# Optimization experiments

Hardware: AMD Instinct MI355X
Metric: run time of the kernel (lower is better)

The kernel has to match this reference:

```python
import jax, jax.numpy as jnp
import numpy as np

NUM_HEADS = 16
EPS = 1e-5


def _ln(x, w, b):
    mu = jnp.mean(x, axis=-1, keepdims=True)
    var = jnp.mean((x - mu) ** 2, axis=-1, keepdims=True)
    return (x - mu) * jax.lax.rsqrt(var + EPS) * w + b


def _ada_ln(x, vol, lw, lb, gamma, beta, vs_w, vs_b):
    y = _ln(x, lw, lb)
    # volatility_scale: Linear(1,1) on vol[..., None] -> sigmoid
    vs = jax.nn.sigmoid(vol[..., None] * vs_w + vs_b)  # (B,S,1)
    return y * (1.0 + vs) * gamma + beta


def setup_inputs() -> dict:
    key = jax.random.key(0)
    ks = jax.random.split(key, 20)
    B, S, H = 8, 1024, 1024
    Hf = 4 * H
    Hg = H // 2
    w = lambda k, i, o: jax.random.normal(k, (i, o), jnp.float32) * 0.02
    inp = {
        'x': jax.random.normal(ks[0], (B, S, H), jnp.float32),
        'volatility': jax.random.uniform(ks[1], (B, S), jnp.float32),
        'Wq': w(ks[2], H, H), 'bq': jnp.zeros((H,), jnp.float32),
        'Wk': w(ks[3], H, H), 'bk': jnp.zeros((H,), jnp.float32),
        'Wv': w(ks[4], H, H), 'bv': jnp.zeros((H,), jnp.float32),
        'Wo': w(ks[5], H, H), 'bo': jnp.zeros((H,), jnp.float32),
        'ln1_w': jnp.ones((H,), jnp.float32), 'ln1_b': jnp.zeros((H,), jnp.float32),
        'gamma1': jnp.ones((), jnp.float32), 'beta1': jnp.zeros((), jnp.float32),
        'vs1_w': jnp.float32(0.3), 'vs1_b': jnp.float32(0.0),
        'ffn_w1': w(ks[6], H, Hf), 'ffn_b1': jnp.zeros((Hf,), jnp.float32),
        'ffn_w2': w(ks[7], Hf, H), 'ffn_b2': jnp.zeros((H,), jnp.float32),
        'gate_w1': w(ks[8], H, Hg), 'gate_b1': jnp.zeros((Hg,), jnp.float32),
        'gate_w2': w(ks[9], Hg, H), 'gate_b2': jnp.zeros((H,), jnp.float32),
        'ln2_w': jnp.ones((H,), jnp.float32), 'ln2_b': jnp.zeros((H,), jnp.float32),
        'gamma2': jnp.ones((), jnp.float32), 'beta2': jnp.zeros((), jnp.float32),
        'vs2_w': jnp.float32(0.3), 'vs2_b': jnp.float32(0.0),
    }
    return inp


def reference(x, volatility, Wq, bq, Wk, bk, Wv, bv, Wo, bo,
              ln1_w, ln1_b, gamma1, beta1, vs1_w, vs1_b,
              ffn_w1, ffn_b1, ffn_w2, ffn_b2,
              gate_w1, gate_b1, gate_w2, gate_b2,
              ln2_w, ln2_b, gamma2, beta2, vs2_w, vs2_b):
    B, S, H = x.shape
    nh = NUM_HEADS
    hd = H // nh
    scale = np.sqrt(hd).astype(np.float32)

    # self-attention (eval mode -> dropout is identity)
    Q = (x @ Wq + bq).reshape(B, S, nh, hd)
    K = (x @ Wk + bk).reshape(B, S, nh, hd)
    V = (x @ Wv + bv).reshape(B, S, nh, hd)
    scores = jnp.einsum('bqhd,bkhd->bhqk', Q, K) / scale
    attn = jax.nn.softmax(scores, axis=-1)
    ctx = jnp.einsum('bhqk,bkhd->bqhd', attn, V).reshape(B, S, H)
    attn_out = ctx @ Wo + bo

    x = x + attn_out
    x = _ada_ln(x, volatility, ln1_w, ln1_b, gamma1, beta1, vs1_w, vs1_b)

    # volatility-adaptive FFN (volatility present -> gated path)
    h = jax.nn.gelu(x @ ffn_w1 + ffn_b1, approximate=False)
    ffn_out = h @ ffn_w2 + ffn_b2
    g = jax.nn.sigmoid(jax.nn.relu(x @ gate_w1 + gate_b1) @ gate_w2 + gate_b2)
    ffn_res = ffn_out * g + x * (1.0 - g)

    x = x + ffn_res
    x = _ada_ln(x, volatility, ln2_w, ln2_b, gamma2, beta2, vs2_w, vs2_b)
    return x
```

## Files before the change

### kernel.cpp

```cpp
#include <hip/hip_runtime.h>
#include <hip/hip_bf16.h>
#include <math.h>


#define HDIM 1024
#define NHEAD 16
#define DHEAD 64
#define NBATCH 8
#define NSEQ 1024
#define NTOK (NBATCH * NSEQ)
#define QKVSTR 3072
#define LNEPS 1e-5f
#define LOG2E_8 0.180336880f

using f32x4 = __attribute__((ext_vector_type(4))) float;
using s16x8 = __attribute__((ext_vector_type(8))) short;
using u16x8 = __attribute__((ext_vector_type(8))) unsigned short;

enum { ACT_NONE = 0, ACT_GELU = 1, ACT_RELU = 2, ACT_SIG = 3 };

__device__ inline float bf2f(unsigned short u) {
    union { unsigned u; float f; } t; t.u = ((unsigned)u) << 16; return t.f;
}
__device__ inline unsigned short f2bf(float f) {
    __hip_bfloat16 h = __float2bfloat16(f);
    return *reinterpret_cast<unsigned short*>(&h);
}
__device__ inline float gelu_f(float t) {
    const float u = t * (0.7978845608f + 0.0356774081f * t * t);
    const float e = __expf(2.f * u);
    const float th = 1.f - 2.f / (e + 1.f);
    return 0.5f * t * (1.f + th);
}

#define GLDS16(g, l) __builtin_amdgcn_global_load_lds( \
    (__attribute__((address_space(1))) void*)(g),      \
    (__attribute__((address_space(3))) void*)(l), 16, 0, 0)
#define MFMA16(a, b, c) __builtin_amdgcn_mfma_f32_16x16x32_bf16(a, b, c, 0, 0, 0)
#define BAR() __builtin_amdgcn_s_barrier()
#define LGKM0() do { asm volatile("s_waitcnt lgkmcnt(0)" ::: "memory"); \
                     __builtin_amdgcn_sched_barrier(0); } while (0)

template<int N> __device__ __forceinline__ void vmwait() {
    asm volatile("s_waitcnt vmcnt(%0)" :: "i"(N) : "memory");
}

__global__ __launch_bounds__(256)
void cast_bf16_k(const float* __restrict__ in, unsigned short* __restrict__ out, int n4)
{
    for (int i = blockIdx.x * 256 + threadIdx.x; i < n4; i += gridDim.x * 256) {
        float4 v = ((const float4*)in)[i];
        ushort4 o;
        o.x = f2bf(v.x); o.y = f2bf(v.y); o.z = f2bf(v.z); o.w = f2bf(v.w);
        ((ushort4*)out)[i] = o;
    }
}

__global__ __launch_bounds__(256)
void concat3_k(const float* __restrict__ a, const float* __restrict__ b,
               const float* __restrict__ c, float* __restrict__ o)
{
    int i = blockIdx.x * 256 + threadIdx.x;
    o[i] = i < 1024 ? a[i] : (i < 2048 ? b[i - 1024] : c[i - 2048]);
}

__global__ __launch_bounds__(256)
void transpose_cast_k(const float* __restrict__ W, unsigned short* __restrict__ Wt,
                      int K, int N)
{
    __shared__ float tile[32][33];
    const int tx = threadIdx.x, ty = threadIdx.y;
    const int k0 = blockIdx.y * 32, n0 = blockIdx.x * 32;
#pragma unroll
    for (int r = 0; r < 32; r += 8)
        tile[ty + r][tx] = W[(size_t)(k0 + ty + r) * N + n0 + tx];
    __syncthreads();
#pragma unroll
    for (int r = 0; r < 32; r += 8)
        Wt[(size_t)(n0 + ty + r) * K + k0 + tx] = f2bf(tile[tx][ty + r]);
}

__global__ __launch_bounds__(256)
void transpose_cast4_k(const float* __restrict__ W0, const float* __restrict__ W1,
                       const float* __restrict__ W2, const float* __restrict__ W3,
                       unsigned short* __restrict__ Wt)
{
    __shared__ float tile[32][33];
    const int z = blockIdx.z;
    const float* W = z == 0 ? W0 : z == 1 ? W1 : z == 2 ? W2 : W3;
    unsigned short* dst = Wt + (size_t)z * HDIM * HDIM;
    const int tx = threadIdx.x, ty = threadIdx.y;
    const int k0 = blockIdx.y * 32, n0 = blockIdx.x * 32;
#pragma unroll
    for (int r = 0; r < 32; r += 8)
        tile[ty + r][tx] = W[(size_t)(k0 + ty + r) * HDIM + n0 + tx];
    __syncthreads();
#pragma unroll
    for (int r = 0; r < 32; r += 8)
        dst[(size_t)(n0 + ty + r) * HDIM + k0 + tx] = f2bf(tile[tx][ty + r]);
}

__global__ __launch_bounds__(256)
void transpose_v_k(const unsigned short* __restrict__ vb, unsigned short* __restrict__ vtb)
{
    __shared__ unsigned short t[64][72];
    const int tid = threadIdx.x;
    const int b = blockIdx.z, h = blockIdx.y;
    const int s0 = blockIdx.x * 64;
    {
        const int r = tid >> 3, c = (tid & 7) * 8;
        *(u16x8*)&t[r][c] =
            *(const u16x8*)&vb[((size_t)(b * NSEQ + s0 + r)) * QKVSTR + h * DHEAD + c];
        *(u16x8*)&t[r + 32][c] =
            *(const u16x8*)&vb[((size_t)(b * NSEQ + s0 + r + 32)) * QKVSTR + h * DHEAD + c];
    }
    __syncthreads();
    {
        const int d = tid & 63, sc = (tid >> 6) * 16;
        u16x8 o0, o1;
#pragma unroll
        for (int i = 0; i < 8; ++i) o0[i] = t[sc + i][d];
#pragma unroll
        for (int i = 0; i < 8; ++i) o1[i] = t[sc + 8 + i][d];
        unsigned short* dst = &vtb[((size_t)((b * NHEAD + h) * DHEAD + d)) * NSEQ + s0 + sc];
        *(u16x8*)dst = o0;
        *(u16x8*)(dst + 8) = o1;
    }
}

template<int ACT, bool HAS_ADD, bool OUT_BF>
__global__ __launch_bounds__(256, 4)
void gemm_hi_k(const unsigned short* __restrict__ A, const unsigned short* __restrict__ Bt,
               const float* __restrict__ bias, const float* __restrict__ add,
               void* __restrict__ Cv, int M, int N, int K, int nbx)
{
    __shared__ alignas(16) unsigned short As[2][128 * 32];
    __shared__ alignas(16) unsigned short Bs[2][128 * 32];

    const int tid = threadIdx.x;
    const int lane = tid & 63;
    const int w = tid >> 6;
    const int wr = w >> 1, wc = w & 1;
    const int chunk = gridDim.x >> 3;
    const int wg = (blockIdx.x & 7) * chunk + (blockIdx.x >> 3);
    const int m0 = (wg / nbx) * 128;
    const int n0 = (wg % nbx) * 128;

    const int fr = lane & 15;
    const int fo = lane >> 4;
    const int fo_swz8 = (fo ^ ((fr >> 1) & 3)) * 8;

    const int srow = tid >> 2;
    const int sg8 = ((tid & 3) ^ ((tid >> 3) & 3)) * 8;

    f32x4 acc[4][4] = {};

    auto stage = [&](int t) {
        const int buf = t & 1;
        const unsigned short* as_ = A + (size_t)(m0 + srow) * K + t * 32 + sg8;
        const unsigned short* bs_ = Bt + (size_t)(n0 + srow) * K + t * 32 + sg8;
        GLDS16(as_, &As[buf][(w * 16) * 32]);
        GLDS16(as_ + (size_t)64 * K, &As[buf][(64 + w * 16) * 32]);
        GLDS16(bs_, &Bs[buf][(w * 16) * 32]);
        GLDS16(bs_ + (size_t)64 * K, &Bs[buf][(64 + w * 16) * 32]);
    };

    const int NT = K / 32;
    stage(0);

    for (int t = 0; t < NT; ++t) {
        if (t + 1 < NT) { stage(t + 1); vmwait<4>(); }
        else            { vmwait<0>(); }
        BAR();

        const int buf = t & 1;
        s16x8 af[4], bf[4];
#pragma unroll
        for (int i = 0; i < 4; ++i)
            af[i] = *(const s16x8*)(&As[buf][(wr * 64 + i * 16 + fr) * 32 + fo_swz8]);
#pragma unroll
        for (int j = 0; j < 4; ++j)
            bf[j] = *(const s16x8*)(&Bs[buf][(wc * 64 + j * 16 + fr) * 32 + fo_swz8]);

        __builtin_amdgcn_s_setprio(1);
#pragma unroll
        for (int i = 0; i < 4; ++i)
#pragma unroll
            for (int j = 0; j < 4; ++j)
                acc[i][j] = MFMA16(af[i], bf[j], acc[i][j]);
        __builtin_amdgcn_s_setprio(0);

        LGKM0();
        BAR();
    }

    float bv[4];
#pragma unroll
    for (int j = 0; j < 4; ++j)
        bv[j] = bias[n0 + wc * 64 + j * 16 + fr];
#pragma unroll
    for (int i = 0; i < 4; ++i) {
#pragma unroll
        for (int j = 0; j < 4; ++j) {
            const int gn = n0 + wc * 64 + j * 16 + fr;
#pragma unroll
            for (int r = 0; r < 4; ++r) {
                const int gm = m0 + wr * 64 + i * 16 + fo * 4 + r;
                float t = acc[i][j][r] + bv[j];
                if (HAS_ADD) t += add[(size_t)gm * N + gn];
                if (ACT == ACT_GELU)      t = gelu_f(t);
                else if (ACT == ACT_RELU) t = fmaxf(t, 0.f);
                else if (ACT == ACT_SIG)  t = 1.f / (1.f + __expf(-t));
                if (OUT_BF) ((unsigned short*)Cv)[(size_t)gm * N + gn] = f2bf(t);
                else        ((float*)Cv)[(size_t)gm * N + gn] = t;
            }
        }
    }
}

__global__ __launch_bounds__(512, 6)
void attn_k(const unsigned short* __restrict__ QKVb, const unsigned short* __restrict__ Vtb,
            unsigned short* __restrict__ Cb)
{
    __shared__ alignas(16) unsigned short Ks[2][64 * 64];
    __shared__ alignas(16) unsigned short Vs[2][64 * 64];
    __shared__ alignas(16) unsigned short Ps[8][16 * 72];

    const int tid = threadIdx.x;
    const int lane = tid & 63;
    const int wid = tid >> 6;
    const int L = blockIdx.x;
    const int xcd = L & 7, s = L >> 3;
    const int bh = xcd + ((s >> 3) << 3);
    const int qt = s & 7;
    const int b = bh >> 4, h = bh & 15;
    const int q0 = qt * 128 + wid * 16;

    const int kcol = lane & 15;
    const int kofs = (lane >> 4) * 8;
    const size_t qoff = ((size_t)(b * NSEQ + q0 + kcol)) * QKVSTR + h * DHEAD + kofs;
    const s16x8 qf0 = *(const s16x8*)(QKVb + qoff);
    const s16x8 qf1 = *(const s16x8*)(QKVb + qoff + 32);

    f32x4 accO[4] = {};
    float mrow[4] = {-1e30f, -1e30f, -1e30f, -1e30f};
    float lsum[4] = {0.f, 0.f, 0.f, 0.f};

    const int lr = lane >> 3;
    const int swz8 = (((lane & 7) ^ lr)) * 8;
    const size_t kbase  = ((size_t)(b * NSEQ)) * QKVSTR + HDIM + h * DHEAD;
    const size_t vtbase = ((size_t)(bh * DHEAD)) * NSEQ;

    unsigned short* const pw = &Ps[wid][0];
    const int prow = (lane >> 4) * 4;

    auto stage = [&](int kt, int buf) {
        const int rowb = wid * 8;
        GLDS16(QKVb + kbase + (size_t)(kt * 64 + rowb + lr) * QKVSTR + swz8,
               Ks[buf] + rowb * 64);
        GLDS16(Vtb + vtbase + (size_t)(rowb + lr) * NSEQ + kt * 64 + swz8,
               Vs[buf] + rowb * 64);
    };

    stage(0, 0);
    asm volatile("s_waitcnt vmcnt(0)" ::: "memory");
    __syncthreads();

    for (int kt = 0; kt < NSEQ / 64; ++kt) {
        const int cur = kt & 1;
        if (kt + 1 < NSEQ / 64) stage(kt + 1, cur ^ 1);

        f32x4 sa[4];
#pragma unroll
        for (int jt = 0; jt < 4; ++jt) {
            const int kr = jt * 16 + kcol;
            const unsigned swz = ((unsigned)(kr & 7)) << 4;
            const s16x8 kf0 = *(const s16x8*)((const char*)Ks[cur] + kr * 128 + ((kofs * 2) ^ swz));
            const s16x8 kf1 = *(const s16x8*)((const char*)Ks[cur] + kr * 128 + ((64 + kofs * 2) ^ swz));
            f32x4 t = {};
            t = MFMA16(qf0, kf0, t);
            t = MFMA16(qf1, kf1, t);
            sa[jt] = t * LOG2E_8;
        }

        float lmax[4];
#pragma unroll
        for (int r = 0; r < 4; ++r)
            lmax[r] = fmaxf(fmaxf(sa[0][r], sa[1][r]), fmaxf(sa[2][r], sa[3][r]));
        const float guard = fmaxf(fmaxf(lmax[0] - mrow[0], lmax[1] - mrow[1]),
                                  fmaxf(lmax[2] - mrow[2], lmax[3] - mrow[3]));
        if (!__all(guard <= 8.f)) {
#pragma unroll
            for (int r = 0; r < 4; ++r) {
                float m = lmax[r];
                m = fmaxf(m, __shfl_xor(m, 1));
                m = fmaxf(m, __shfl_xor(m, 2));
                m = fmaxf(m, __shfl_xor(m, 4));
                m = fmaxf(m, __shfl_xor(m, 8));
                const float mn = fmaxf(mrow[r], m);
                const float corr = exp2f(mrow[r] - mn);
                mrow[r] = mn;
                lsum[r] *= corr;
#pragma unroll
                for (int dt = 0; dt < 4; ++dt) accO[dt][r] *= corr;
            }
        }
#pragma unroll
        for (int r = 0; r < 4; ++r) {
#pragma unroll
            for (int jt = 0; jt < 4; ++jt) {
                const float p = exp2f(sa[jt][r] - mrow[r]);
                pw[(prow + r) * 72 + jt * 16 + kcol] = f2bf(p);
                lsum[r] += p;
            }
        }

#pragma unroll
        for (int kc = 0; kc < 2; ++kc) {
            const s16x8 pa = *(const s16x8*)(pw + kcol * 72 + kc * 32 + kofs);
#pragma unroll
            for (int dt = 0; dt < 4; ++dt) {
                const int dr = dt * 16 + kcol;
                const unsigned swz = ((unsigned)(dr & 7)) << 4;
                const s16x8 vf = *(const s16x8*)((const char*)Vs[cur] + dr * 128 +
                                                 ((kc * 64 + kofs * 2) ^ swz));
                accO[dt] = MFMA16(pa, vf, accO[dt]);
            }
        }

        if (kt + 1 < NSEQ / 64) asm volatile("s_waitcnt vmcnt(0)" ::: "memory");
        __builtin_amdgcn_s_barrier();
    }

#pragma unroll
    for (int r = 0; r < 4; ++r) {
        lsum[r] += __shfl_xor(lsum[r], 1);
        lsum[r] += __shfl_xor(lsum[r], 2);
        lsum[r] += __shfl_xor(lsum[r], 4);
        lsum[r] += __shfl_xor(lsum[r], 8);
    }

    const size_t obase = ((size_t)(b * NSEQ + q0 + prow)) * HDIM + h * DHEAD;
#pragma unroll
    for (int r = 0; r < 4; ++r) {
        const float rl = 1.f / lsum[r];
#pragma unroll
        for (int dt = 0; dt < 4; ++dt)
            Cb[obase + (size_t)r * HDIM + dt * 16 + kcol] = f2bf(accO[dt][r] * rl);
    }
}

template<int MODE, bool WRITE_BF>
__global__ __launch_bounds__(256)
void adaln_k(const float* __restrict__ a, const float* __restrict__ fo,
             const float* __restrict__ g, const float* __restrict__ vol,
             const float* __restrict__ lw, const float* __restrict__ lb,
             const float* __restrict__ gm, const float* __restrict__ bt,
             const float* __restrict__ vsw, const float* __restrict__ vsb,
             float* __restrict__ out, unsigned short* __restrict__ out_bf)
{
    const int tok = blockIdx.x;
    const int tid = threadIdx.x;
    const size_t base = (size_t)tok * HDIM + tid * 4;
    float v[4];
    {
        float4 va = *(const float4*)&a[base];
        if (MODE == 1) {
            float4 vf = *(const float4*)&fo[base];
            float4 vg = *(const float4*)&g[base];
            v[0] = va.x * (2.f - vg.x) + vf.x * vg.x;
            v[1] = va.y * (2.f - vg.y) + vf.y * vg.y;
            v[2] = va.z * (2.f - vg.z) + vf.z * vg.z;
            v[3] = va.w * (2.f - vg.w) + vf.w * vg.w;
        } else {
            v[0] = va.x; v[1] = va.y; v[2] = va.z; v[3] = va.w;
        }
    }
    float sum = v[0] + v[1] + v[2] + v[3];
    float sq  = v[0]*v[0] + v[1]*v[1] + v[2]*v[2] + v[3]*v[3];
#pragma unroll
    for (int off = 32; off > 0; off >>= 1) {
        sum += __shfl_down(sum, off);
        sq  += __shfl_down(sq, off);
    }
    __shared__ float ssum[4], ssq[4];
    const int wid = tid >> 6, lane = tid & 63;
    if (lane == 0) { ssum[wid] = sum; ssq[wid] = sq; }
    __syncthreads();
    const float tsum = ssum[0] + ssum[1] + ssum[2] + ssum[3];
    const float tsq  = ssq[0]  + ssq[1]  + ssq[2]  + ssq[3];
    const float mu   = tsum * (1.f / 1024.f);
    const float var  = tsq * (1.f / 1024.f) - mu * mu;
    const float rstd = rsqrtf(var + LNEPS);
    const float vsv  = 1.f / (1.f + __expf(-(vol[tok] * vsw[0] + vsb[0])));
    const float sca  = (1.f + vsv) * gm[0];
    const float off2 = bt[0];
    const float4 lwv = *(const float4*)&lw[tid * 4];
    const float4 lbv = *(const float4*)&lb[tid * 4];
    float r0 = ((v[0] - mu) * rstd * lwv.x + lbv.x) * sca + off2;
    float r1 = ((v[1] - mu) * rstd * lwv.y + lbv.y) * sca + off2;
    float r2 = ((v[2] - mu) * rstd * lwv.z + lbv.z) * sca + off2;
    float r3 = ((v[3] - mu) * rstd * lwv.w + lbv.w) * sca + off2;
    *(float4*)&out[base] = make_float4(r0, r1, r2, r3);
    if (WRITE_BF) {
        ushort4 ob;
        ob.x = f2bf(r0); ob.y = f2bf(r1); ob.z = f2bf(r2); ob.w = f2bf(r3);
        *(ushort4*)&out_bf[base] = ob;
    }
}

extern "C" void kernel_launch(void* const* d_in, const int* in_sizes, int n_in,
                              void* d_out, int out_size, void* d_ws, size_t ws_size,
                              hipStream_t stream)
{
    (void)in_sizes; (void)n_in; (void)out_size; (void)ws_size;
    const float* x    = (const float*)d_in[0];
    const float* vol  = (const float*)d_in[1];
    const float* Wq   = (const float*)d_in[2];  const float* bq  = (const float*)d_in[3];
    const float* Wk   = (const float*)d_in[4];  const float* bk  = (const float*)d_in[5];
    const float* Wv   = (const float*)d_in[6];  const float* bv  = (const float*)d_in[7];
    const float* Wo   = (const float*)d_in[8];  const float* bo  = (const float*)d_in[9];
    const float* ln1w = (const float*)d_in[10]; const float* ln1b = (const float*)d_in[11];
    const float* gm1  = (const float*)d_in[12]; const float* be1 = (const float*)d_in[13];
    const float* vs1w = (const float*)d_in[14]; const float* vs1b = (const float*)d_in[15];
    const float* fw1  = (const float*)d_in[16]; const float* fb1 = (const float*)d_in[17];
    const float* fw2  = (const float*)d_in[18]; const float* fb2 = (const float*)d_in[19];
    const float* gw1  = (const float*)d_in[20]; const float* gb1 = (const float*)d_in[21];
    const float* gw2  = (const float*)d_in[22]; const float* gb2 = (const float*)d_in[23];
    const float* ln2w = (const float*)d_in[24]; const float* ln2b = (const float*)d_in[25];
    const float* gm2  = (const float*)d_in[26]; const float* be2 = (const float*)d_in[27];
    const float* vs2w = (const float*)d_in[28]; const float* vs2b = (const float*)d_in[29];

    char* w = (char*)d_ws;
    auto MB = [](size_t v) { return v << 20; };
    unsigned short* wtqkv = (unsigned short*)(w + MB(0));
    unsigned short* wto   = (unsigned short*)(w + MB(6));
    unsigned short* wtf1  = (unsigned short*)(w + MB(8));
    unsigned short* wtf2  = (unsigned short*)(w + MB(16));
    unsigned short* wtg1  = (unsigned short*)(w + MB(24));
    unsigned short* wtg2  = (unsigned short*)(w + MB(25));
    unsigned short* xb   = (unsigned short*)(w + MB(26));
    unsigned short* qkvb = (unsigned short*)(w + MB(42));
    unsigned short* vtb  = (unsigned short*)(w + MB(90));
    unsigned short* cxb  = (unsigned short*)(w + MB(106));
    float*          ao   = (float*)(w + MB(122));
    float*          x1   = (float*)(w + MB(42));
    unsigned short* x1b  = (unsigned short*)(w + MB(74));
    unsigned short* hb   = (unsigned short*)(w + MB(90));
    float*          ffn  = (float*)(w + MB(154));
    unsigned short* ghb  = (unsigned short*)(w + MB(26));
    float*          gg   = (float*)(w + MB(90));
    float*          bqkv = (float*)(w + MB(186));

    dim3 blk(256);
    dim3 tb(32, 8);
    transpose_cast4_k<<<dim3(32, 32, 4), tb, 0, stream>>>(Wq, Wk, Wv, Wo, wtqkv);
    transpose_cast_k<<<dim3(4096/32, 1024/32), tb, 0, stream>>>(fw1, wtf1, 1024, 4096);
    transpose_cast_k<<<dim3(1024/32, 4096/32), tb, 0, stream>>>(fw2, wtf2, 4096, 1024);
    transpose_cast_k<<<dim3(512/32, 1024/32),  tb, 0, stream>>>(gw1, wtg1, 1024, 512);
    transpose_cast_k<<<dim3(1024/32, 512/32),  tb, 0, stream>>>(gw2, wtg2, 512, 1024);
    cast_bf16_k<<<2048, blk, 0, stream>>>(x, xb, NTOK * HDIM / 4);
    concat3_k<<<12, blk, 0, stream>>>(bq, bk, bv, bqkv);

    gemm_hi_k<ACT_NONE, false, true><<<dim3(24 * 64), blk, 0, stream>>>(
        xb, wtqkv, bqkv, nullptr, qkvb, NTOK, QKVSTR, HDIM, 24);
    transpose_v_k<<<dim3(NSEQ / 64, NHEAD, NBATCH), blk, 0, stream>>>(qkvb + 2048, vtb);
    attn_k<<<dim3(1024), 512, 0, stream>>>(qkvb, vtb, cxb);
    gemm_hi_k<ACT_NONE, true, false><<<dim3(8 * 64), blk, 0, stream>>>(
        cxb, wto, bo, x, ao, NTOK, HDIM, HDIM, 8);
    adaln_k<0, true><<<dim3(NTOK), blk, 0, stream>>>(
        ao, nullptr, nullptr, vol, ln1w, ln1b, gm1, be1, vs1w, vs1b, x1, x1b);
    gemm_hi_k<ACT_GELU, false, true><<<dim3(32 * 64), blk, 0, stream>>>(
        x1b, wtf1, fb1, nullptr, hb, NTOK, 4096, HDIM, 32);
    gemm_hi_k<ACT_NONE, false, false><<<dim3(8 * 64), blk, 0, stream>>>(
        hb, wtf2, fb2, nullptr, ffn, NTOK, HDIM, 4096, 8);
    gemm_hi_k<ACT_RELU, false, true><<<dim3(4 * 64), blk, 0, stream>>>(
        x1b, wtg1, gb1, nullptr, ghb, NTOK, 512, HDIM, 4);
    gemm_hi_k<ACT_SIG, false, false><<<dim3(8 * 64), blk, 0, stream>>>(
        ghb, wtg2, gb2, nullptr, gg, NTOK, HDIM, 512, 8);
    adaln_k<1, false><<<dim3(NTOK), blk, 0, stream>>>(
        x1, ffn, gg, vol, ln2w, ln2b, gm2, be2, vs2w, vs2b, (float*)d_out, nullptr);
}
```

Before: 469.4 us.

## Fuse FFN-up and gate-up GEMMs, store FFN and gate outputs in bf16

```diff
diff --git a/kernel.cpp b/kernel.cpp
--- a/kernel.cpp
+++ b/kernel.cpp
@@ -17,7 +17,7 @@
 using s16x8 = __attribute__((ext_vector_type(8))) short;
 using u16x8 = __attribute__((ext_vector_type(8))) unsigned short;
 
-enum { ACT_NONE = 0, ACT_GELU = 1, ACT_RELU = 2, ACT_SIG = 3 };
+enum { ACT_NONE = 0, ACT_GELU = 1, ACT_RELU = 2, ACT_SIG = 3, ACT_GR = 4 };
 
 __device__ inline float bf2f(unsigned short u) {
     union { unsigned u; float f; } t; t.u = ((unsigned)u) << 16; return t.f;
@@ -62,6 +62,14 @@
 {
     int i = blockIdx.x * 256 + threadIdx.x;
     o[i] = i < 1024 ? a[i] : (i < 2048 ? b[i - 1024] : c[i - 2048]);
+}
+
+__global__ __launch_bounds__(256)
+void concat2_k(const float* __restrict__ a, const float* __restrict__ b,
+               float* __restrict__ o)
+{
+    int i = blockIdx.x * 256 + threadIdx.x;
+    o[i] = i < 4096 ? a[i] : b[i - 4096];
 }
 
 __global__ __launch_bounds__(256)
@@ -129,10 +137,10 @@
 }
 
 template<int ACT, bool HAS_ADD, bool OUT_BF>
-__global__ __launch_bounds__(256, 4)
+__global__ __launch_bounds__(256, 5)
 void gemm_hi_k(const unsigned short* __restrict__ A, const unsigned short* __restrict__ Bt,
                const float* __restrict__ bias, const float* __restrict__ add,
-               void* __restrict__ Cv, int M, int N, int K, int nbx)
+               void* __restrict__ Cv, int M, int N, int K, int lda, int nbx)
 {
     __shared__ alignas(16) unsigned short As[2][128 * 32];
     __shared__ alignas(16) unsigned short Bs[2][128 * 32];
@@ -157,10 +165,10 @@
 
     auto stage = [&](int t) {
         const int buf = t & 1;
-        const unsigned short* as_ = A + (size_t)(m0 + srow) * K + t * 32 + sg8;
+        const unsigned short* as_ = A + (size_t)(m0 + srow) * lda + t * 32 + sg8;
         const unsigned short* bs_ = Bt + (size_t)(n0 + srow) * K + t * 32 + sg8;
         GLDS16(as_, &As[buf][(w * 16) * 32]);
-        GLDS16(as_ + (size_t)64 * K, &As[buf][(64 + w * 16) * 32]);
+        GLDS16(as_ + (size_t)64 * lda, &As[buf][(64 + w * 16) * 32]);
         GLDS16(bs_, &Bs[buf][(w * 16) * 32]);
         GLDS16(bs_ + (size_t)64 * K, &Bs[buf][(64 + w * 16) * 32]);
     };
@@ -211,6 +219,7 @@
                 if (ACT == ACT_GELU)      t = gelu_f(t);
                 else if (ACT == ACT_RELU) t = fmaxf(t, 0.f);
                 else if (ACT == ACT_SIG)  t = 1.f / (1.f + __expf(-t));
+                else if (ACT == ACT_GR)   t = (gn < 4096) ? gelu_f(t) : fmaxf(t, 0.f);
                 if (OUT_BF) ((unsigned short*)Cv)[(size_t)gm * N + gn] = f2bf(t);
                 else        ((float*)Cv)[(size_t)gm * N + gn] = t;
             }
@@ -352,8 +361,10 @@
 
 template<int MODE, bool WRITE_BF>
 __global__ __launch_bounds__(256)
-void adaln_k(const float* __restrict__ a, const float* __restrict__ fo,
-             const float* __restrict__ g, const float* __restrict__ vol,
+void adaln_k(const float* __restrict__ a,
+             const unsigned short* __restrict__ fo_bf,
+             const unsigned short* __restrict__ g_bf,
+             const float* __restrict__ vol,
              const float* __restrict__ lw, const float* __restrict__ lb,
              const float* __restrict__ gm, const float* __restrict__ bt,
              const float* __restrict__ vsw, const float* __restrict__ vsb,
@@ -366,12 +377,14 @@
     {
         float4 va = *(const float4*)&a[base];
         if (MODE == 1) {
-            float4 vf = *(const float4*)&fo[base];
-            float4 vg = *(const float4*)&g[base];
-            v[0] = va.x * (2.f - vg.x) + vf.x * vg.x;
-            v[1] = va.y * (2.f - vg.y) + vf.y * vg.y;
-            v[2] = va.z * (2.f - vg.z) + vf.z * vg.z;
-            v[3] = va.w * (2.f - vg.w) + vf.w * vg.w;
+            ushort4 uf = *(const ushort4*)&fo_bf[base];
+            ushort4 ug = *(const ushort4*)&g_bf[base];
+            float f0 = bf2f(uf.x), f1 = bf2f(uf.y), f2 = bf2f(uf.z), f3 = bf2f(uf.w);
+            float g0 = bf2f(ug.x), g1 = bf2f(ug.y), g2 = bf2f(ug.z), g3 = bf2f(ug.w);
+            v[0] = va.x * (2.f - g0) + f0 * g0;
+            v[1] = va.y * (2.f - g1) + f1 * g1;
+            v[2] = va.z * (2.f - g2) + f2 * g2;
+            v[3] = va.w * (2.f - g3) + f3 * g3;
         } else {
             v[0] = va.x; v[1] = va.y; v[2] = va.z; v[3] = va.w;
         }
@@ -435,9 +448,9 @@
     auto MB = [](size_t v) { return v << 20; };
     unsigned short* wtqkv = (unsigned short*)(w + MB(0));
     unsigned short* wto   = (unsigned short*)(w + MB(6));
-    unsigned short* wtf1  = (unsigned short*)(w + MB(8));
-    unsigned short* wtf2  = (unsigned short*)(w + MB(16));
-    unsigned short* wtg1  = (unsigned short*)(w + MB(24));
+    unsigned short* wtfg  = (unsigned short*)(w + MB(8));
+    unsigned short* wtg1  = (unsigned short*)(w + MB(16));
+    unsigned short* wtf2  = (unsigned short*)(w + MB(17));
     unsigned short* wtg2  = (unsigned short*)(w + MB(25));
     unsigned short* xb   = (unsigned short*)(w + MB(26));
     unsigned short* qkvb = (unsigned short*)(w + MB(42));
@@ -446,38 +459,37 @@
     float*          ao   = (float*)(w + MB(122));
     float*          x1   = (float*)(w + MB(42));
     unsigned short* x1b  = (unsigned short*)(w + MB(74));
-    unsigned short* hb   = (unsigned short*)(w + MB(90));
-    float*          ffn  = (float*)(w + MB(154));
-    unsigned short* ghb  = (unsigned short*)(w + MB(26));
-    float*          gg   = (float*)(w + MB(90));
-    float*          bqkv = (float*)(w + MB(186));
+    unsigned short* hgb  = (unsigned short*)(w + MB(90));
+    unsigned short* ffnb = (unsigned short*)(w + MB(162));
+    unsigned short* ggb  = (unsigned short*)(w + MB(26));
+    float*          bqkv = (float*)(w + MB(184));
+    float*          bfg  = (float*)(w + MB(185));
 
     dim3 blk(256);
     dim3 tb(32, 8);
     transpose_cast4_k<<<dim3(32, 32, 4), tb, 0, stream>>>(Wq, Wk, Wv, Wo, wtqkv);
-    transpose_cast_k<<<dim3(4096/32, 1024/32), tb, 0, stream>>>(fw1, wtf1, 1024, 4096);
+    transpose_cast_k<<<dim3(4096/32, 1024/32), tb, 0, stream>>>(fw1, wtfg, 1024, 4096);
+    transpose_cast_k<<<dim3(512/32, 1024/32),  tb, 0, stream>>>(gw1, wtg1, 1024, 512);
     transpose_cast_k<<<dim3(1024/32, 4096/32), tb, 0, stream>>>(fw2, wtf2, 4096, 1024);
-    transpose_cast_k<<<dim3(512/32, 1024/32),  tb, 0, stream>>>(gw1, wtg1, 1024, 512);
     transpose_cast_k<<<dim3(1024/32, 512/32),  tb, 0, stream>>>(gw2, wtg2, 512, 1024);
     cast_bf16_k<<<2048, blk, 0, stream>>>(x, xb, NTOK * HDIM / 4);
     concat3_k<<<12, blk, 0, stream>>>(bq, bk, bv, bqkv);
+    concat2_k<<<18, blk, 0, stream>>>(fb1, gb1, bfg);
 
     gemm_hi_k<ACT_NONE, false, true><<<dim3(24 * 64), blk, 0, stream>>>(
-        xb, wtqkv, bqkv, nullptr, qkvb, NTOK, QKVSTR, HDIM, 24);
+        xb, wtqkv, bqkv, nullptr, qkvb, NTOK, QKVSTR, HDIM, HDIM, 24);
     transpose_v_k<<<dim3(NSEQ / 64, NHEAD, NBATCH), blk, 0, stream>>>(qkvb + 2048, vtb);
     attn_k<<<dim3(1024), 512, 0, stream>>>(qkvb, vtb, cxb);
     gemm_hi_k<ACT_NONE, true, false><<<dim3(8 * 64), blk, 0, stream>>>(
-        cxb, wto, bo, x, ao, NTOK, HDIM, HDIM, 8);
+        cxb, wto, bo, x, ao, NTOK, HDIM, HDIM, HDIM, 8);
     adaln_k<0, true><<<dim3(NTOK), blk, 0, stream>>>(
         ao, nullptr, nullptr, vol, ln1w, ln1b, gm1, be1, vs1w, vs1b, x1, x1b);
-    gemm_hi_k<ACT_GELU, false, true><<<dim3(32 * 64), blk, 0, stream>>>(
-        x1b, wtf1, fb1, nullptr, hb, NTOK, 4096, HDIM, 32);
-    gemm_hi_k<ACT_NONE, false, false><<<dim3(8 * 64), blk, 0, stream>>>(
-        hb, wtf2, fb2, nullptr, ffn, NTOK, HDIM, 4096, 8);
-    gemm_hi_k<ACT_RELU, false, true><<<dim3(4 * 64), blk, 0, stream>>>(
-        x1b, wtg1, gb1, nullptr, ghb, NTOK, 512, HDIM, 4);
-    gemm_hi_k<ACT_SIG, false, false><<<dim3(8 * 64), blk, 0, stream>>>(
-        ghb, wtg2, gb2, nullptr, gg, NTOK, HDIM, 512, 8);
+    gemm_hi_k<ACT_GR, false, true><<<dim3(36 * 64), blk, 0, stream>>>(
+        x1b, wtfg, bfg, nullptr, hgb, NTOK, 4608, HDIM, HDIM, 36);
+    gemm_hi_k<ACT_NONE, false, true><<<dim3(8 * 64), blk, 0, stream>>>(
+        hgb, wtf2, fb2, nullptr, ffnb, NTOK, HDIM, 4096, 4608, 8);
+    gemm_hi_k<ACT_SIG, false, true><<<dim3(8 * 64), blk, 0, stream>>>(
+        hgb + 4096, wtg2, gb2, nullptr, ggb, NTOK, HDIM, 512, 4608, 8);
     adaln_k<1, false><<<dim3(NTOK), blk, 0, stream>>>(
-        x1, ffn, gg, vol, ln2w, ln2b, gm2, be2, vs2w, vs2b, (float*)d_out, nullptr);
-}
+        x1, ffnb, ggb, vol, ln2w, ln2b, gm2, be2, vs2w, vs2b, (float*)d_out, nullptr);
+}
```

New measurement: 686.9 us. +46.3%, slower.

## Use 64-row GEMM tiles for narrow-N GEMMs and store FFN/gate outputs as bf16

Applied to the files above, without the earlier changes.

```diff
diff --git a/kernel.cpp b/kernel.cpp
--- a/kernel.cpp
+++ b/kernel.cpp
@@ -128,22 +128,26 @@
     }
 }
 
-template<int ACT, bool HAS_ADD, bool OUT_BF>
+template<int BM, int ACT, bool HAS_ADD, bool OUT_BF>
 __global__ __launch_bounds__(256, 4)
 void gemm_hi_k(const unsigned short* __restrict__ A, const unsigned short* __restrict__ Bt,
                const float* __restrict__ bias, const float* __restrict__ add,
                void* __restrict__ Cv, int M, int N, int K, int nbx)
 {
-    __shared__ alignas(16) unsigned short As[2][128 * 32];
+    constexpr int NREP = (BM == 128) ? 4 : 2;
+    constexpr int AR = BM / 64;
+    constexpr int VM = AR + 2;
+    __shared__ alignas(16) unsigned short As[2][BM * 32];
     __shared__ alignas(16) unsigned short Bs[2][128 * 32];
 
     const int tid = threadIdx.x;
     const int lane = tid & 63;
     const int w = tid >> 6;
-    const int wr = w >> 1, wc = w & 1;
+    const int wr = (BM == 128) ? (w >> 1) : 0;
+    const int wcb = (BM == 128) ? ((w & 1) * 64) : (w * 32);
     const int chunk = gridDim.x >> 3;
     const int wg = (blockIdx.x & 7) * chunk + (blockIdx.x >> 3);
-    const int m0 = (wg / nbx) * 128;
+    const int m0 = (wg / nbx) * BM;
     const int n0 = (wg % nbx) * 128;
 
     const int fr = lane & 15;
@@ -153,14 +157,15 @@
     const int srow = tid >> 2;
     const int sg8 = ((tid & 3) ^ ((tid >> 3) & 3)) * 8;
 
-    f32x4 acc[4][4] = {};
+    f32x4 acc[4][NREP] = {};
 
     auto stage = [&](int t) {
         const int buf = t & 1;
         const unsigned short* as_ = A + (size_t)(m0 + srow) * K + t * 32 + sg8;
         const unsigned short* bs_ = Bt + (size_t)(n0 + srow) * K + t * 32 + sg8;
         GLDS16(as_, &As[buf][(w * 16) * 32]);
-        GLDS16(as_ + (size_t)64 * K, &As[buf][(64 + w * 16) * 32]);
+        if constexpr (BM == 128)
+            GLDS16(as_ + (size_t)64 * K, &As[buf][(64 + w * 16) * 32]);
         GLDS16(bs_, &Bs[buf][(w * 16) * 32]);
         GLDS16(bs_ + (size_t)64 * K, &Bs[buf][(64 + w * 16) * 32]);
     };
@@ -169,24 +174,24 @@
     stage(0);
 
     for (int t = 0; t < NT; ++t) {
-        if (t + 1 < NT) { stage(t + 1); vmwait<4>(); }
+        if (t + 1 < NT) { stage(t + 1); vmwait<VM>(); }
         else            { vmwait<0>(); }
         BAR();
 
         const int buf = t & 1;
-        s16x8 af[4], bf[4];
+        s16x8 af[4], bf[NREP];
 #pragma unroll
         for (int i = 0; i < 4; ++i)
             af[i] = *(const s16x8*)(&As[buf][(wr * 64 + i * 16 + fr) * 32 + fo_swz8]);
 #pragma unroll
-        for (int j = 0; j < 4; ++j)
-            bf[j] = *(const s16x8*)(&Bs[buf][(wc * 64 + j * 16 + fr) * 32 + fo_swz8]);
+        for (int j = 0; j < NREP; ++j)
+            bf[j] = *(const s16x8*)(&Bs[buf][(wcb + j * 16 + fr) * 32 + fo_swz8]);
 
         __builtin_amdgcn_s_setprio(1);
 #pragma unroll
         for (int i = 0; i < 4; ++i)
 #pragma unroll
-            for (int j = 0; j < 4; ++j)
+            for (int j = 0; j < NREP; ++j)
                 acc[i][j] = MFMA16(af[i], bf[j], acc[i][j]);
         __builtin_amdgcn_s_setprio(0);
 
@@ -194,15 +199,15 @@
         BAR();
     }
 
-    float bv[4];
-#pragma unroll
-    for (int j = 0; j < 4; ++j)
-        bv[j] = bias[n0 + wc * 64 + j * 16 + fr];
+    float bv[NREP];
+#pragma unroll
+    for (int j = 0; j < NREP; ++j)
+        bv[j] = bias[n0 + wcb + j * 16 + fr];
 #pragma unroll
     for (int i = 0; i < 4; ++i) {
 #pragma unroll
-        for (int j = 0; j < 4; ++j) {
-            const int gn = n0 + wc * 64 + j * 16 + fr;
+        for (int j = 0; j < NREP; ++j) {
+            const int gn = n0 + wcb + j * 16 + fr;
 #pragma unroll
             for (int r = 0; r < 4; ++r) {
                 const int gm = m0 + wr * 64 + i * 16 + fo * 4 + r;
@@ -352,8 +357,10 @@
 
 template<int MODE, bool WRITE_BF>
 __global__ __launch_bounds__(256)
-void adaln_k(const float* __restrict__ a, const float* __restrict__ fo,
-             const float* __restrict__ g, const float* __restrict__ vol,
+void adaln_k(const float* __restrict__ a,
+             const unsigned short* __restrict__ fo_bf,
+             const unsigned short* __restrict__ g_bf,
+             const float* __restrict__ vol,
              const float* __restrict__ lw, const float* __restrict__ lb,
              const float* __restrict__ gm, const float* __restrict__ bt,
              const float* __restrict__ vsw, const float* __restrict__ vsb,
@@ -366,12 +373,14 @@
     {
         float4 va = *(const float4*)&a[base];
         if (MODE == 1) {
-            float4 vf = *(const float4*)&fo[base];
-            float4 vg = *(const float4*)&g[base];
-            v[0] = va.x * (2.f - vg.x) + vf.x * vg.x;
-            v[1] = va.y * (2.f - vg.y) + vf.y * vg.y;
-            v[2] = va.z * (2.f - vg.z) + vf.z * vg.z;
-            v[3] = va.w * (2.f - vg.w) + vf.w * vg.w;
+            ushort4 uf = *(const ushort4*)&fo_bf[base];
+            ushort4 ug = *(const ushort4*)&g_bf[base];
+            float f0 = bf2f(uf.x), f1 = bf2f(uf.y), f2 = bf2f(uf.z), f3 = bf2f(uf.w);
+            float g0 = bf2f(ug.x), g1 = bf2f(ug.y), g2 = bf2f(ug.z), g3 = bf2f(ug.w);
+            v[0] = va.x * (2.f - g0) + f0 * g0;
+            v[1] = va.y * (2.f - g1) + f1 * g1;
+            v[2] = va.z * (2.f - g2) + f2 * g2;
+            v[3] = va.w * (2.f - g3) + f3 * g3;
         } else {
             v[0] = va.x; v[1] = va.y; v[2] = va.z; v[3] = va.w;
         }
@@ -447,10 +456,10 @@
     float*          x1   = (float*)(w + MB(42));
     unsigned short* x1b  = (unsigned short*)(w + MB(74));
     unsigned short* hb   = (unsigned short*)(w + MB(90));
-    float*          ffn  = (float*)(w + MB(154));
-    unsigned short* ghb  = (unsigned short*)(w + MB(26));
-    float*          gg   = (float*)(w + MB(90));
-    float*          bqkv = (float*)(w + MB(186));
+    unsigned short* ffnb = (unsigned short*)(w + MB(154));
+    unsigned short* ghb  = (unsigned short*)(w + MB(170));
+    unsigned short* ggb  = (unsigned short*)(w + MB(26));
+    float*          bqkv = (float*)(w + MB(184));
 
     dim3 blk(256);
     dim3 tb(32, 8);
@@ -462,22 +471,22 @@
     cast_bf16_k<<<2048, blk, 0, stream>>>(x, xb, NTOK * HDIM / 4);
     concat3_k<<<12, blk, 0, stream>>>(bq, bk, bv, bqkv);
 
-    gemm_hi_k<ACT_NONE, false, true><<<dim3(24 * 64), blk, 0, stream>>>(
+    gemm_hi_k<128, ACT_NONE, false, true><<<dim3(24 * 64), blk, 0, stream>>>(
         xb, wtqkv, bqkv, nullptr, qkvb, NTOK, QKVSTR, HDIM, 24);
     transpose_v_k<<<dim3(NSEQ / 64, NHEAD, NBATCH), blk, 0, stream>>>(qkvb + 2048, vtb);
     attn_k<<<dim3(1024), 512, 0, stream>>>(qkvb, vtb, cxb);
-    gemm_hi_k<ACT_NONE, true, false><<<dim3(8 * 64), blk, 0, stream>>>(
+    gemm_hi_k<64, ACT_NONE, true, false><<<dim3(128 * 8), blk, 0, stream>>>(
         cxb, wto, bo, x, ao, NTOK, HDIM, HDIM, 8);
     adaln_k<0, true><<<dim3(NTOK), blk, 0, stream>>>(
         ao, nullptr, nullptr, vol, ln1w, ln1b, gm1, be1, vs1w, vs1b, x1, x1b);
-    gemm_hi_k<ACT_GELU, false, true><<<dim3(32 * 64), blk, 0, stream>>>(
+    gemm_hi_k<128, ACT_GELU, false, true><<<dim3(32 * 64), blk, 0, stream>>>(
         x1b, wtf1, fb1, nullptr, hb, NTOK, 4096, HDIM, 32);
-    gemm_hi_k<ACT_NONE, false, false><<<dim3(8 * 64), blk, 0, stream>>>(
-        hb, wtf2, fb2, nullptr, ffn, NTOK, HDIM, 4096, 8);
-    gemm_hi_k<ACT_RELU, false, true><<<dim3(4 * 64), blk, 0, stream>>>(
+    gemm_hi_k<64, ACT_NONE, false, true><<<dim3(128 * 8), blk, 0, stream>>>(
+        hb, wtf2, fb2, nullptr, ffnb, NTOK, HDIM, 4096, 8);
+    gemm_hi_k<64, ACT_RELU, false, true><<<dim3(128 * 4), blk, 0, stream>>>(
         x1b, wtg1, gb1, nullptr, ghb, NTOK, 512, HDIM, 4);
-    gemm_hi_k<ACT_SIG, false, false><<<dim3(8 * 64), blk, 0, stream>>>(
-        ghb, wtg2, gb2, nullptr, gg, NTOK, HDIM, 512, 8);
+    gemm_hi_k<64, ACT_SIG, false, true><<<dim3(128 * 8), blk, 0, stream>>>(
+        ghb, wtg2, gb2, nullptr, ggb, NTOK, HDIM, 512, 8);
     adaln_k<1, false><<<dim3(NTOK), blk, 0, stream>>>(
-        x1, ffn, gg, vol, ln2w, ln2b, gm2, be2, vs2w, vs2b, (float*)d_out, nullptr);
-}
+        x1, ffnb, ggb, vol, ln2w, ln2b, gm2, be2, vs2w, vs2b, (float*)d_out, nullptr);
+}
```

After: 463.9 us. About the same (-1.2%).
